# Kernel tuning notes

Hardware: AMD Instinct MI355X
Metric: run time of the kernel (lower is better)

## Reference

```python
import jax, jax.numpy as jnp
import numpy as np

H = 64   # hidden_size
K = 20   # number of attention groups


def _gru_layer(x, Wih, Whh, bih, bhh):
    # x: [B, T, I] -> [B, T, H]; PyTorch GRU gate order (r, z, n)
    xw = x @ Wih.T + bih  # [B, T, 3H]
    h0 = jnp.zeros((x.shape[0], Whh.shape[1]), x.dtype)

    def step(h, xt):
        gh = h @ Whh.T + bhh
        xr, xz, xn = jnp.split(xt, 3, axis=-1)
        hr, hz, hn = jnp.split(gh, 3, axis=-1)
        r = jax.nn.sigmoid(xr + hr)
        z = jax.nn.sigmoid(xz + hz)
        n = jnp.tanh(xn + r * hn)
        h = (1.0 - z) * n + z * h
        return h, h

    _, hs = jax.lax.scan(step, h0, jnp.swapaxes(xw, 0, 1))
    return jnp.swapaxes(hs, 0, 1)


def setup_inputs():
    key = jax.random.key(0)
    ks = iter(jax.random.split(key, 40))

    def p(shape, fan_in):
        s = 1.0 / np.sqrt(fan_in)
        return jax.random.uniform(next(ks), shape, jnp.float32, -s, s)

    N, T, D = 10240, 60, 6  # N = K * m with m = 512
    inp = {"x": jax.random.normal(next(ks), (N, T, D), jnp.float32)}
    inp.update(
        rnn_Wih0=p((3 * H, D), D), rnn_Whh0=p((3 * H, H), H),
        rnn_bih0=p((3 * H,), H), rnn_bhh0=p((3 * H,), H),
        rnn_Wih1=p((3 * H, H), H), rnn_Whh1=p((3 * H, H), H),
        rnn_bih1=p((3 * H,), H), rnn_bhh1=p((3 * H,), H),
        trans_W=p((H, H), H), trans_b=p((H,), H),
        a=jax.random.normal(next(ks), (2 * H, 1), jnp.float32),
        fc_W=p((H, H), H), fc_b=p((H,), H),
        fco_W=p((1, H), H), fco_b=p((1,), H),
        al_in_W=p((H, H), H), al_in_b=p((H,), H),
        al_Wih0=p((3 * H, H), H), al_Whh0=p((3 * H, H), H),
        al_bih0=p((3 * H,), H), al_bhh0=p((3 * H,), H),
        al_Wih1=p((3 * H, H), H), al_Whh1=p((3 * H, H), H),
        al_bih1=p((3 * H,), H), al_bhh1=p((3 * H,), H),
        al_att1_W=p((H // 2, H), H), al_att1_b=p((H // 2,), H),
        al_att2_W=p((1, H // 2), H // 2),
        al_out_W=p((1, 2 * H), 2 * H), al_out_b=p((1,), 2 * H),
    )
    return inp


def reference(x, rnn_Wih0, rnn_Whh0, rnn_bih0, rnn_bhh0,
              rnn_Wih1, rnn_Whh1, rnn_bih1, rnn_bhh1,
              trans_W, trans_b, a, fc_W, fc_b, fco_W, fco_b,
              al_in_W, al_in_b,
              al_Wih0, al_Whh0, al_bih0, al_bhh0,
              al_Wih1, al_Whh1, al_bih1, al_bhh1,
              al_att1_W, al_att1_b, al_att2_W, al_out_W, al_out_b):
    # ---- 2-layer GRU encoder over time ----
    out = _gru_layer(x, rnn_Wih0, rnn_Whh0, rnn_bih0, rnn_bhh0)
    out = _gru_layer(out, rnn_Wih1, rnn_Whh1, rnn_bih1, rnn_bhh1)
    h = out[:, -1, :].reshape(K, -1, H)  # [K, m, H]

    # ---- dense all-pairs GAT attention (split-projection form of a^T [x_j ; x_i]) ----
    xp = h @ trans_W.T + trans_b         # transformation(x) == transformation(y)
    s_dst = xp @ a[:H, 0]                # contributes along column index j
    s_src = xp @ a[H:, 0]                # contributes along row index i
    score = jax.nn.leaky_relu(s_src[:, :, None] + s_dst[:, None, :])  # [K, m, m]
    att = jax.nn.softmax(score, axis=2)
    h = jnp.einsum('kij,kjd->kid', att, h) + h
    h = h @ fc_W.T + fc_b
    h = jnp.swapaxes(h, 0, 1)            # [m, K, H]  (K acts as seq len for ALSTM)

    # ---- ALSTM (inference: dropout inactive) ----
    z = jnp.tanh(h @ al_in_W.T + al_in_b)
    r = _gru_layer(z, al_Wih0, al_Whh0, al_bih0, al_bhh0)
    r = _gru_layer(r, al_Wih1, al_Whh1, al_bih1, al_bhh1)
    att_s = jax.nn.softmax(jnp.tanh(r @ al_att1_W.T + al_att1_b) @ al_att2_W.T, axis=1)  # [m, K, 1]
    out_att = jnp.sum(r * att_s, axis=1)
    alstm_out = (jnp.concatenate([r[:, -1, :], out_att], axis=1) @ al_out_W.T + al_out_b)[:, 0]

    pred = (jax.nn.leaky_relu(h[:, -1, :]) @ fco_W.T + fco_b)[:, 0]
    return (alstm_out, pred)
```

## Files before the change

### kernel.cpp

```cpp
#include <hip/hip_runtime.h>

#define DEV __device__ __forceinline__

DEV float fast_rcp(float x) {
#if __has_builtin(__builtin_amdgcn_rcpf)
  return __builtin_amdgcn_rcpf(x);
#else
  return 1.0f / x;
#endif
}
DEV float sigm(float x) { return fast_rcp(1.0f + __expf(-x)); }
DEV float tanh_f(float x) {
  float e = __expf(-2.0f * fabsf(x));
  float t = 1.0f - 2.0f * e * fast_rcp(1.0f + e);
  return copysignf(t, x);
}
DEV float lrelu(float x) { return x > 0.0f ? x : 0.01f * x; }

DEV float wave_sum(float v) {
#pragma unroll
  for (int m = 32; m; m >>= 1) v += __shfl_xor(v, m);
  return v;
}
DEV float wave_max(float v) {
#pragma unroll
  for (int m = 32; m; m >>= 1) v = fmaxf(v, __shfl_xor(v, m));
  return v;
}
DEV float dot4(float4 w, float4 x, float acc) {
  acc = fmaf(w.x, x.x, acc);
  acc = fmaf(w.y, x.y, acc);
  acc = fmaf(w.z, x.z, acc);
  acc = fmaf(w.w, x.w, acc);
  return acc;
}

DEV float bcast(float v, int lane) {
  return __int_as_float(__builtin_amdgcn_readlane(__float_as_int(v), lane));
}

constexpr int E_SPW = 5;
constexpr int E_WAVES = 8;
constexpr int L_W0 = 0;
constexpr int L_W1 = 12288;
constexpr int E_DW = 36864;
constexpr int E_LDS = E_DW * 4;

#define DOT_BATCH8(WBASE, KB, HREG, AN)                                   \
  {                                                                       \
    float wv_[8][3];                                                      \
    float hh_[8][E_SPW];                                                  \
    _Pragma("unroll") for (int u = 0; u < 8; ++u) {                       \
      const int k_ = (KB) * 8 + u;                                        \
      const int wb_ = (WBASE) + k_ * 192 + j3;                            \
      wv_[u][0] = lds[wb_];                                               \
      wv_[u][1] = lds[wb_ + 1];                                           \
      wv_[u][2] = lds[wb_ + 2];                                           \
      _Pragma("unroll") for (int s = 0; s < E_SPW; ++s)                   \
        hh_[u][s] = bcast(HREG[s], k_);                                   \
    }                                                                     \
    _Pragma("unroll") for (int u = 0; u < 8; ++u) {                       \
      _Pragma("unroll") for (int s = 0; s < E_SPW; ++s) {                 \
        ar[s] = fmaf(wv_[u][0], hh_[u][s], ar[s]);                        \
        az[s] = fmaf(wv_[u][1], hh_[u][s], az[s]);                        \
        AN[s] = fmaf(wv_[u][2], hh_[u][s], AN[s]);                        \
      }                                                                   \
    }                                                                     \
  }

__launch_bounds__(512)
__global__ void gru2_enc(const float* __restrict__ x,
                         const float* __restrict__ w3e0,
                         const float* __restrict__ w3e1,
                         const float* __restrict__ bih0, const float* __restrict__ bhh0,
                         const float* __restrict__ bih1, const float* __restrict__ bhh1,
                         float* __restrict__ h_out) {
  extern __shared__ float lds[];
  const int tid = threadIdx.x;
  const int wave = tid >> 6;
  const int j = tid & 63;
  const int j3 = j * 3;

  {
    const float4* s0 = (const float4*)(w3e0 + 6 * 192);
    for (int i = tid; i < 12288 / 4; i += 512) ((float4*)(lds + L_W0))[i] = s0[i];
    const float4* s1 = (const float4*)w3e1;
    for (int i = tid; i < 24576 / 4; i += 512) ((float4*)(lds + L_W1))[i] = s1[i];
  }
  float wx0[6][3];
#pragma unroll
  for (int k = 0; k < 6; ++k)
#pragma unroll
    for (int g = 0; g < 3; ++g) wx0[k][g] = w3e0[k * 192 + j3 + g];

  const float br0 = bih0[j] + bhh0[j];
  const float bz0 = bih0[64 + j] + bhh0[64 + j];
  const float bxn0 = bih0[128 + j];
  const float bhn0 = bhh0[128 + j];
  const float br1 = bih1[j] + bhh1[j];
  const float bz1 = bih1[64 + j] + bhh1[64 + j];
  const float bxn1 = bih1[128 + j];
  const float bhn1 = bhh1[128 + j];

  float h0r[E_SPW], h1r[E_SPW];
#pragma unroll
  for (int s = 0; s < E_SPW; ++s) { h0r[s] = 0.0f; h1r[s] = 0.0f; }
  __syncthreads();

  const int seq0 = blockIdx.x * (E_WAVES * E_SPW) + wave * E_SPW;
  const int si = j / 6;
  const int ci = j - si * 6;
  const bool xlane = (j < 6 * E_SPW);
  const float* xg = x + (size_t)(seq0 + si) * 360 + ci;

  float xcur = xlane ? xg[0] : 0.0f;

  for (int t = 0; t < 60; ++t) {
    float xnext = (xlane && t + 1 < 60) ? xg[(size_t)(t + 1) * 6] : 0.0f;

    float ar[E_SPW], az[E_SPW], anx[E_SPW], anh[E_SPW];
#pragma unroll
    for (int s = 0; s < E_SPW; ++s) { ar[s] = 0.f; az[s] = 0.f; anx[s] = 0.f; anh[s] = 0.f; }

#pragma clang loop unroll(disable)
    for (int kb = 0; kb < 8; ++kb) DOT_BATCH8(L_W0, kb, h0r, anh)

    {
      float xk_[E_SPW][6];
#pragma unroll
      for (int s = 0; s < E_SPW; ++s)
#pragma unroll
        for (int c = 0; c < 6; ++c) xk_[s][c] = bcast(xcur, s * 6 + c);
#pragma unroll
      for (int s = 0; s < E_SPW; ++s)
#pragma unroll
        for (int c = 0; c < 6; ++c) {
          ar[s] = fmaf(wx0[c][0], xk_[s][c], ar[s]);
          az[s] = fmaf(wx0[c][1], xk_[s][c], az[s]);
          anx[s] = fmaf(wx0[c][2], xk_[s][c], anx[s]);
        }
    }
#pragma unroll
    for (int s = 0; s < E_SPW; ++s) {
      float r = sigm(ar[s] + br0);
      float z = sigm(az[s] + bz0);
      float n = tanh_f(anx[s] + bxn0 + r * (anh[s] + bhn0));
      h0r[s] = (1.0f - z) * n + z * h0r[s];
    }

#pragma unroll
    for (int s = 0; s < E_SPW; ++s) { ar[s] = 0.f; az[s] = 0.f; anx[s] = 0.f; anh[s] = 0.f; }
#pragma clang loop unroll(disable)
    for (int kb = 0; kb < 8; ++kb) DOT_BATCH8(L_W1, kb, h0r, anx)
#pragma clang loop unroll(disable)
    for (int kb = 0; kb < 8; ++kb) DOT_BATCH8(L_W1 + 64 * 192, kb, h1r, anh)
#pragma unroll
    for (int s = 0; s < E_SPW; ++s) {
      float r = sigm(ar[s] + br1);
      float z = sigm(az[s] + bz1);
      float n = tanh_f(anx[s] + bxn1 + r * (anh[s] + bhn1));
      h1r[s] = (1.0f - z) * n + z * h1r[s];
    }
    xcur = xnext;
  }

#pragma unroll
  for (int s = 0; s < E_SPW; ++s)
    h_out[(size_t)(seq0 + s) * 64 + j] = h1r[s];
}

constexpr int A_W_DW = 128 * 192;
constexpr int A_WAVES = 8;
constexpr int A_LDS = (A_W_DW + A_WAVES * 128) * 4;

__launch_bounds__(512, 2)
__global__ void gru1(const float* __restrict__ xin,
                     const float* __restrict__ w3,
                     const float* __restrict__ bih, const float* __restrict__ bhh,
                     int T,
                     float* __restrict__ rout) {
  extern __shared__ float lds[];
  const int tid = threadIdx.x;
  const int wave = tid >> 6;
  const int j = tid & 63;
  const int j3 = j * 3;
  const int XB = A_W_DW + wave * 128;

  {
    const float4* sp = (const float4*)w3;
    for (int i = tid; i < A_W_DW / 4; i += 512) ((float4*)lds)[i] = sp[i];
  }
  const float br = bih[j] + bhh[j];
  const float bz = bih[64 + j] + bhh[64 + j];
  const float bxn = bih[128 + j];
  const float bhn = bhh[128 + j];

  float hr = 0.0f;
  lds[XB + 64 + j] = 0.0f;
  __syncthreads();

  const int seq = blockIdx.x * A_WAVES + wave;
  const float* xs = xin + (size_t)seq * T * 64;

#define A_QUAD(WROW0, HOFF, AN)                                            \
  {                                                                        \
    float4 hv = *(const float4*)&lds[XB + (HOFF)];                         \
    _Pragma("unroll") for (int c = 0; c < 4; ++c) {                        \
      const float wr = lds[((WROW0) + c) * 192 + j3];                      \
      const float wz = lds[((WROW0) + c) * 192 + j3 + 1];                  \
      const float wn = lds[((WROW0) + c) * 192 + j3 + 2];                  \
      const float hc = (c == 0) ? hv.x : (c == 1) ? hv.y                   \
                      : (c == 2) ? hv.z : hv.w;                            \
      ar = fmaf(wr, hc, ar);                                               \
      az = fmaf(wz, hc, az);                                               \
      AN = fmaf(wn, hc, AN);                                               \
    }                                                                      \
  }

  float xcur = xs[j];
  for (int t = 0; t < T; ++t) {
    float xnext = (t + 1 < T) ? xs[(size_t)(t + 1) * 64 + j] : 0.0f;
    lds[XB + j] = xcur;

    float ar = 0.f, az = 0.f, anx = 0.f, anh = 0.f;
#pragma unroll
    for (int kq = 0; kq < 16; ++kq) A_QUAD(kq * 4, kq * 4, anx);
#pragma unroll
    for (int kq = 0; kq < 16; ++kq) A_QUAD(64 + kq * 4, 64 + kq * 4, anh);

    float r = sigm(ar + br);
    float z = sigm(az + bz);
    float n = tanh_f(anx + bxn + r * (anh + bhn));
    float h = (1.0f - z) * n + z * hr;
    hr = h;
    lds[XB + 64 + j] = h;
    rout[((size_t)seq * T + t) * 64 + j] = h;
    xcur = xnext;
  }
#undef A_QUAD
}

__global__ void w3_prep(const float* __restrict__ Wih0, const float* __restrict__ Whh0,
                        const float* __restrict__ Wih1, const float* __restrict__ Whh1,
                        const float* __restrict__ aWih0, const float* __restrict__ aWhh0,
                        const float* __restrict__ aWih1, const float* __restrict__ aWhh1,
                        float* __restrict__ d_e0, float* __restrict__ d_e1,
                        float* __restrict__ d_a0, float* __restrict__ d_a1) {
  const int sec = blockIdx.x >> 3;
  const int bi = blockIdx.x & 7;
  const float* Wih; const float* Whh; float* dst; int I;
  if (sec == 0)      { Wih = Wih0;  Whh = Whh0;  dst = d_e0; I = 6; }
  else if (sec == 1) { Wih = Wih1;  Whh = Whh1;  dst = d_e1; I = 64; }
  else if (sec == 2) { Wih = aWih0; Whh = aWhh0; dst = d_a0; I = 64; }
  else               { Wih = aWih1; Whh = aWhh1; dst = d_a1; I = 64; }
  const int tot = (I + 64) * 192;
  for (int idx = bi * blockDim.x + threadIdx.x; idx < tot; idx += 8 * blockDim.x) {
    const int k = idx / 192;
    const int rem = idx - k * 192;
    const int jj = rem / 3;
    const int g = rem - jj * 3;
    dst[idx] = (k < I) ? Wih[(g * 64 + jj) * I + k] : Whh[(g * 64 + jj) * 64 + (k - I)];
  }
}

__global__ void gat_prep(const float* __restrict__ tW, const float* __restrict__ tb,
                         const float* __restrict__ a, float* __restrict__ vbuf) {
  const int d = threadIdx.x;
  float vd = 0.0f, vs = 0.0f;
  for (int e = 0; e < 64; ++e) {
    float w = tW[e * 64 + d];
    vd = fmaf(w, a[e], vd);
    vs = fmaf(w, a[64 + e], vs);
  }
  vbuf[d] = vd;
  vbuf[64 + d] = vs;
  if (d == 0) {
    float cd = 0.0f, cs = 0.0f;
    for (int e = 0; e < 64; ++e) {
      cd = fmaf(tb[e], a[e], cd);
      cs = fmaf(tb[e], a[64 + e], cs);
    }
    vbuf[128] = cd;
    vbuf[129] = cs;
  }
}

__global__ void gat_svals(const float* __restrict__ h_enc, const float* __restrict__ vbuf,
                          float* __restrict__ s_src, float* __restrict__ s_dst) {
  const int wave = (blockIdx.x * blockDim.x + threadIdx.x) >> 6;
  const int lane = threadIdx.x & 63;
  float h = h_enc[(size_t)wave * 64 + lane];
  float pd = h * vbuf[lane];
  float ps = h * vbuf[64 + lane];
  pd = wave_sum(pd);
  ps = wave_sum(ps);
  if (lane == 0) {
    s_dst[wave] = pd + vbuf[128];
    s_src[wave] = ps + vbuf[129];
  }
}

__launch_bounds__(256)
__global__ void gat_attn(const float* __restrict__ h_enc,
                         const float* __restrict__ s_src,
                         const float* __restrict__ s_dst,
                         float* __restrict__ hout) {
  const int k = blockIdx.x >> 7;
  const int tile = blockIdx.x & 127;
  const int wv = threadIdx.x >> 6;
  const int lane = threadIdx.x & 63;
  const int i = tile * 4 + wv;
  __shared__ float sdbuf[512];
  __shared__ __align__(16) float pbuf[4][512];

  for (int u = threadIdx.x; u < 512; u += 256) sdbuf[u] = s_dst[k * 512 + u];
  __syncthreads();

  const float si = s_src[k * 512 + i];
  float ev[8];
  float mx = -1e30f;
#pragma unroll
  for (int u = 0; u < 8; ++u) {
    ev[u] = lrelu(si + sdbuf[lane + u * 64]);
    mx = fmaxf(mx, ev[u]);
  }
  mx = wave_max(mx);
  float lsum = 0.0f;
#pragma unroll
  for (int u = 0; u < 8; ++u) {
    float p = __expf(ev[u] - mx);
    pbuf[wv][lane + u * 64] = p;
    lsum += p;
  }
  lsum = wave_sum(lsum);
  const float inv = fast_rcp(lsum);

  const float* hk = h_enc + (size_t)k * 512 * 64;
  const float4* pv = (const float4*)pbuf[wv];
  float acc0 = 0.0f, acc1 = 0.0f;
#pragma unroll 2
  for (int jj = 0; jj < 128; ++jj) {
    float4 p = pv[jj];
    const float* hp = hk + (size_t)(jj * 4) * 64 + lane;
    acc0 = fmaf(p.x, hp[0], acc0);
    acc1 = fmaf(p.y, hp[64], acc1);
    acc0 = fmaf(p.z, hp[128], acc0);
    acc1 = fmaf(p.w, hp[192], acc1);
  }
  hout[((size_t)k * 512 + i) * 64 + lane] =
      (acc0 + acc1) * inv + hk[(size_t)i * 64 + lane];
}

__launch_bounds__(256)
__global__ void gat_out(const float* __restrict__ hin,
                        const float* __restrict__ fcW, const float* __restrict__ fcb,
                        const float* __restrict__ fcoW, const float* __restrict__ fcob,
                        const float* __restrict__ alinW, const float* __restrict__ alinb,
                        float* __restrict__ zout, float* __restrict__ pred) {
  const int wv = threadIdx.x >> 6;
  const int lane = threadIdx.x & 63;
  const int n = blockIdx.x * 4 + wv;
  const int k = n >> 9;
  const int i = n & 511;
  __shared__ __align__(16) float rbuf[4][64];
  __shared__ __align__(16) float rbuf2[4][64];

  float4 fw[16], aw[16];
  {
    const float4* p1 = (const float4*)(fcW + lane * 64);
    const float4* p2 = (const float4*)(alinW + lane * 64);
#pragma unroll
    for (int kk = 0; kk < 16; ++kk) fw[kk] = p1[kk];
#pragma unroll
    for (int kk = 0; kk < 16; ++kk) aw[kk] = p2[kk];
  }

  rbuf[wv][lane] = hin[(size_t)n * 64 + lane];
  float h2 = fcb[lane];
  const float4* rv = (const float4*)rbuf[wv];
#pragma unroll
  for (int kk = 0; kk < 16; ++kk) h2 = dot4(fw[kk], rv[kk], h2);

  if (k == 19) {
    float pv = lrelu(h2) * fcoW[lane];
    pv = wave_sum(pv);
    if (lane == 0) pred[i] = pv + fcob[0];
  }

  rbuf2[wv][lane] = h2;
  float zz = alinb[lane];
  const float4* rv2 = (const float4*)rbuf2[wv];
#pragma unroll
  for (int kk = 0; kk < 16; ++kk) zz = dot4(aw[kk], rv2[kk], zz);
  zout[((size_t)i * 20 + k) * 64 + lane] = tanh_f(zz);
}

__launch_bounds__(256)
__global__ void alstm_head(const float* __restrict__ r1,
                           const float* __restrict__ W1,
                           const float* __restrict__ b1,
                           const float* __restrict__ W2,
                           const float* __restrict__ Wo,
                           const float* __restrict__ bo,
                           float* __restrict__ alstm_out) {
  const int wv = threadIdx.x >> 6;
  const int lane = threadIdx.x & 63;
  const int i = blockIdx.x * 4 + wv;
  const int e = lane & 31;
  __shared__ __align__(16) float rbuf[4][64];
  __shared__ float scb[4][20];

  float4 w1r[16];
  {
    const float4* p = (const float4*)(W1 + e * 64);
#pragma unroll
    for (int kk = 0; kk < 16; ++kk) w1r[kk] = p[kk];
  }
  const float b1e = b1[e];
  const float w2e = W2[e];

  for (int k = 0; k < 20; ++k) {
    rbuf[wv][lane] = r1[((size_t)i * 20 + k) * 64 + lane];
    float u = b1e;
    const float4* rp = (const float4*)rbuf[wv];
#pragma unroll
    for (int kk = 0; kk < 16; ++kk) u = dot4(w1r[kk], rp[kk], u);
    u = tanh_f(u) * w2e;
#pragma unroll
    for (int m = 16; m; m >>= 1) u += __shfl_xor(u, m);
    if (lane == 0) scb[wv][k] = u;
  }

  float mx = -1e30f;
#pragma unroll
  for (int k = 0; k < 20; ++k) mx = fmaxf(mx, scb[wv][k]);
  float p[20];
  float l = 0.0f;
#pragma unroll
  for (int k = 0; k < 20; ++k) {
    p[k] = __expf(scb[wv][k] - mx);
    l += p[k];
  }
  const float inv = fast_rcp(l);

  float oa = 0.0f, rlast = 0.0f;
#pragma unroll
  for (int k = 0; k < 20; ++k) {
    float rv = r1[((size_t)i * 20 + k) * 64 + lane];
    oa = fmaf(p[k], rv, oa);
    if (k == 19) rlast = rv;
  }
  oa *= inv;
  float v = fmaf(Wo[lane], rlast, Wo[64 + lane] * oa);
  v = wave_sum(v);
  if (lane == 0) alstm_out[i] = v + bo[0];
}

extern "C" void kernel_launch(void* const* d_in, const int* in_sizes, int n_in,
                              void* d_out, int out_size, void* d_ws, size_t ws_size,
                              hipStream_t stream) {
  const float* x      = (const float*)d_in[0];
  const float* Wih0   = (const float*)d_in[1];
  const float* Whh0   = (const float*)d_in[2];
  const float* bih0   = (const float*)d_in[3];
  const float* bhh0   = (const float*)d_in[4];
  const float* Wih1   = (const float*)d_in[5];
  const float* Whh1   = (const float*)d_in[6];
  const float* bih1   = (const float*)d_in[7];
  const float* bhh1   = (const float*)d_in[8];
  const float* transW = (const float*)d_in[9];
  const float* transb = (const float*)d_in[10];
  const float* a_vec  = (const float*)d_in[11];
  const float* fcW    = (const float*)d_in[12];
  const float* fcb    = (const float*)d_in[13];
  const float* fcoW   = (const float*)d_in[14];
  const float* fcob   = (const float*)d_in[15];
  const float* alinW  = (const float*)d_in[16];
  const float* alinb  = (const float*)d_in[17];
  const float* aWih0  = (const float*)d_in[18];
  const float* aWhh0  = (const float*)d_in[19];
  const float* abih0  = (const float*)d_in[20];
  const float* abhh0  = (const float*)d_in[21];
  const float* aWih1  = (const float*)d_in[22];
  const float* aWhh1  = (const float*)d_in[23];
  const float* abih1  = (const float*)d_in[24];
  const float* abhh1  = (const float*)d_in[25];
  const float* att1W  = (const float*)d_in[26];
  const float* att1b  = (const float*)d_in[27];
  const float* att2W  = (const float*)d_in[28];
  const float* aloutW = (const float*)d_in[29];
  const float* aloutb = (const float*)d_in[30];

  float* out = (float*)d_out;

  float* W = (float*)d_ws;
  float* h_enc = W; W += 10240 * 64;
  float* vbuf  = W; W += 256;
  float* s_src = W; W += 10240;
  float* s_dst = W; W += 10240;
  float* hout  = W; W += 10240 * 64;
  float* zbuf  = W; W += 512 * 20 * 64;
  float* r1    = W; W += 512 * 20 * 64;
  float* w3a0  = W; W += 24576;
  float* w3a1  = W; W += 24576;
  float* w3e0 = zbuf;
  float* w3e1 = zbuf + 13440;

  static bool attr_done = false;
  if (!attr_done) {
    hipFuncSetAttribute((const void*)gru2_enc,
                        hipFuncAttributeMaxDynamicSharedMemorySize, E_LDS);
    hipFuncSetAttribute((const void*)gru1,
                        hipFuncAttributeMaxDynamicSharedMemorySize, A_LDS);
    attr_done = true;
  }

  w3_prep<<<32, 256, 0, stream>>>(Wih0, Whh0, Wih1, Whh1, aWih0, aWhh0,
                                  aWih1, aWhh1, w3e0, w3e1, w3a0, w3a1);
  gru2_enc<<<256, 512, E_LDS, stream>>>(x, w3e0, w3e1, bih0, bhh0, bih1,
                                        bhh1, h_enc);
  gat_prep<<<1, 64, 0, stream>>>(transW, transb, a_vec, vbuf);
  gat_svals<<<2560, 256, 0, stream>>>(h_enc, vbuf, s_src, s_dst);
  gat_attn<<<2560, 256, 0, stream>>>(h_enc, s_src, s_dst, hout);
  gat_out<<<2560, 256, 0, stream>>>(hout, fcW, fcb, fcoW, fcob, alinW, alinb,
                                    zbuf, out + 512);
  gru1<<<64, 512, A_LDS, stream>>>(zbuf, w3a0, abih0, abhh0, 20, h_enc);
  gru1<<<64, 512, A_LDS, stream>>>(h_enc, w3a1, abih1, abhh1, 20, r1);
  alstm_head<<<128, 256, 0, stream>>>(r1, att1W, att1b, att2W, aloutW, aloutb,
                                      out);
}
```

Baseline: 1.421 ms.

## Replace readlane broadcasts with DPP wave rotation in encoder GRU matvecs

```diff
diff --git a/kernel.cpp b/kernel.cpp
--- a/kernel.cpp
+++ b/kernel.cpp
@@ -39,34 +39,18 @@
   return __int_as_float(__builtin_amdgcn_readlane(__float_as_int(v), lane));
 }
 
+DEV float rot1(float v) {
+  const int i = __float_as_int(v);
+  return __int_as_float(
+      __builtin_amdgcn_update_dpp(i, i, 0x13C, 0xF, 0xF, true));
+}
+
 constexpr int E_SPW = 5;
 constexpr int E_WAVES = 8;
 constexpr int L_W0 = 0;
 constexpr int L_W1 = 12288;
 constexpr int E_DW = 36864;
 constexpr int E_LDS = E_DW * 4;
-
-#define DOT_BATCH8(WBASE, KB, HREG, AN)                                   \
-  {                                                                       \
-    float wv_[8][3];                                                      \
-    float hh_[8][E_SPW];                                                  \
-    _Pragma("unroll") for (int u = 0; u < 8; ++u) {                       \
-      const int k_ = (KB) * 8 + u;                                        \
-      const int wb_ = (WBASE) + k_ * 192 + j3;                            \
-      wv_[u][0] = lds[wb_];                                               \
-      wv_[u][1] = lds[wb_ + 1];                                           \
-      wv_[u][2] = lds[wb_ + 2];                                           \
-      _Pragma("unroll") for (int s = 0; s < E_SPW; ++s)                   \
-        hh_[u][s] = bcast(HREG[s], k_);                                   \
-    }                                                                     \
-    _Pragma("unroll") for (int u = 0; u < 8; ++u) {                       \
-      _Pragma("unroll") for (int s = 0; s < E_SPW; ++s) {                 \
-        ar[s] = fmaf(wv_[u][0], hh_[u][s], ar[s]);                        \
-        az[s] = fmaf(wv_[u][1], hh_[u][s], az[s]);                        \
-        AN[s] = fmaf(wv_[u][2], hh_[u][s], AN[s]);                        \
-      }                                                                   \
-    }                                                                     \
-  }
 
 __launch_bounds__(512)
 __global__ void gru2_enc(const float* __restrict__ x,
@@ -122,8 +106,22 @@
 #pragma unroll
     for (int s = 0; s < E_SPW; ++s) { ar[s] = 0.f; az[s] = 0.f; anx[s] = 0.f; anh[s] = 0.f; }
 
-#pragma clang loop unroll(disable)
-    for (int kb = 0; kb < 8; ++kb) DOT_BATCH8(L_W0, kb, h0r, anh)
+    {
+      float c0 = h0r[0], c1 = h0r[1], c2 = h0r[2], c3 = h0r[3], c4 = h0r[4];
+      int krel = j;
+#pragma clang loop unroll_count(4)
+      for (int r = 0; r < 64; ++r) {
+        const int wb = L_W0 + krel * 192 + j3;
+        const float wr = lds[wb], wz = lds[wb + 1], wn = lds[wb + 2];
+        ar[0] = fmaf(wr, c0, ar[0]); az[0] = fmaf(wz, c0, az[0]); anh[0] = fmaf(wn, c0, anh[0]);
+        ar[1] = fmaf(wr, c1, ar[1]); az[1] = fmaf(wz, c1, az[1]); anh[1] = fmaf(wn, c1, anh[1]);
+        ar[2] = fmaf(wr, c2, ar[2]); az[2] = fmaf(wz, c2, az[2]); anh[2] = fmaf(wn, c2, anh[2]);
+        ar[3] = fmaf(wr, c3, ar[3]); az[3] = fmaf(wz, c3, az[3]); anh[3] = fmaf(wn, c3, anh[3]);
+        ar[4] = fmaf(wr, c4, ar[4]); az[4] = fmaf(wz, c4, az[4]); anh[4] = fmaf(wn, c4, anh[4]);
+        c0 = rot1(c0); c1 = rot1(c1); c2 = rot1(c2); c3 = rot1(c3); c4 = rot1(c4);
+        krel = (krel - 1) & 63;
+      }
+    }
 
     {
       float xk_[E_SPW][6];
@@ -150,10 +148,32 @@
 
 #pragma unroll
     for (int s = 0; s < E_SPW; ++s) { ar[s] = 0.f; az[s] = 0.f; anx[s] = 0.f; anh[s] = 0.f; }
-#pragma clang loop unroll(disable)
-    for (int kb = 0; kb < 8; ++kb) DOT_BATCH8(L_W1, kb, h0r, anx)
-#pragma clang loop unroll(disable)
-    for (int kb = 0; kb < 8; ++kb) DOT_BATCH8(L_W1 + 64 * 192, kb, h1r, anh)
+
+    {
+      float a0 = h0r[0], a1 = h0r[1], a2 = h0r[2], a3 = h0r[3], a4 = h0r[4];
+      float b0 = h1r[0], b1 = h1r[1], b2 = h1r[2], b3 = h1r[3], b4 = h1r[4];
+      int krel = j;
+#pragma clang loop unroll_count(2)
+      for (int r = 0; r < 64; ++r) {
+        const int wbx = L_W1 + krel * 192 + j3;
+        const int wbh = wbx + 64 * 192;
+        const float wrx = lds[wbx], wzx = lds[wbx + 1], wnx = lds[wbx + 2];
+        const float wrh = lds[wbh], wzh = lds[wbh + 1], wnh = lds[wbh + 2];
+        ar[0] = fmaf(wrx, a0, ar[0]); az[0] = fmaf(wzx, a0, az[0]); anx[0] = fmaf(wnx, a0, anx[0]);
+        ar[1] = fmaf(wrx, a1, ar[1]); az[1] = fmaf(wzx, a1, az[1]); anx[1] = fmaf(wnx, a1, anx[1]);
+        ar[2] = fmaf(wrx, a2, ar[2]); az[2] = fmaf(wzx, a2, az[2]); anx[2] = fmaf(wnx, a2, anx[2]);
+        ar[3] = fmaf(wrx, a3, ar[3]); az[3] = fmaf(wzx, a3, az[3]); anx[3] = fmaf(wnx, a3, anx[3]);
+        ar[4] = fmaf(wrx, a4, ar[4]); az[4] = fmaf(wzx, a4, az[4]); anx[4] = fmaf(wnx, a4, anx[4]);
+        ar[0] = fmaf(wrh, b0, ar[0]); az[0] = fmaf(wzh, b0, az[0]); anh[0] = fmaf(wnh, b0, anh[0]);
+        ar[1] = fmaf(wrh, b1, ar[1]); az[1] = fmaf(wzh, b1, az[1]); anh[1] = fmaf(wnh, b1, anh[1]);
+        ar[2] = fmaf(wrh, b2, ar[2]); az[2] = fmaf(wzh, b2, az[2]); anh[2] = fmaf(wnh, b2, anh[2]);
+        ar[3] = fmaf(wrh, b3, ar[3]); az[3] = fmaf(wzh, b3, az[3]); anh[3] = fmaf(wnh, b3, anh[3]);
+        ar[4] = fmaf(wrh, b4, ar[4]); az[4] = fmaf(wzh, b4, az[4]); anh[4] = fmaf(wnh, b4, anh[4]);
+        a0 = rot1(a0); a1 = rot1(a1); a2 = rot1(a2); a3 = rot1(a3); a4 = rot1(a4);
+        b0 = rot1(b0); b1 = rot1(b1); b2 = rot1(b2); b3 = rot1(b3); b4 = rot1(b4);
+        krel = (krel - 1) & 63;
+      }
+    }
 #pragma unroll
     for (int s = 0; s < E_SPW; ++s) {
       float r = sigm(ar[s] + br1);
```

Result: faster. 1.246 ms (-12.3%).
